# Kernel optimization log

Hardware: AMD Instinct MI355X
Metric: run time of the kernel (lower is better)

## Reference

```python
import math
import jax, jax.numpy as jnp
import numpy as np

E = 256
HEADS = 8
WS = 8
BN_EPS = 1e-5


def pos_encoding_2d(embed_dim, H, W):
    d_half = embed_dim // 2
    div = jnp.exp(jnp.arange(0, d_half, 2, dtype=jnp.float32) * (-math.log(10000.0) / d_half))
    ang_h = jnp.arange(H, dtype=jnp.float32)[:, None] * div[None, :]  # [H, d_half//2]
    pe_h = jnp.zeros((H, d_half), jnp.float32).at[:, 0::2].set(jnp.sin(ang_h)).at[:, 1::2].set(jnp.cos(ang_h))
    ang_w = jnp.arange(W, dtype=jnp.float32)[:, None] * div[None, :]
    pe_w = jnp.zeros((W, d_half), jnp.float32).at[:, 0::2].set(jnp.sin(ang_w)).at[:, 1::2].set(jnp.cos(ang_w))
    pe = jnp.concatenate([
        jnp.broadcast_to(pe_h[:, None, :], (H, W, d_half)),
        jnp.broadcast_to(pe_w[None, :, :], (H, W, d_half)),
    ], axis=-1)  # [H, W, E]
    return jnp.transpose(pe, (2, 0, 1))[None]  # [1, E, H, W]


def window_partition(x, ws):
    # x: [B, E, H, W] -> [B*Hn*Wn, ws*ws, E]
    B, e, H, W = x.shape
    Hn, Wn = H // ws, W // ws
    x = x.reshape(B, e, Hn, ws, Wn, ws)
    x = jnp.transpose(x, (0, 2, 4, 3, 5, 1))  # [B, Hn, Wn, ws, ws, E]
    return x.reshape(B * Hn * Wn, ws * ws, e)


def window_reverse(x, B, H, W, ws):
    Hn, Wn = H // ws, W // ws
    e = x.shape[-1]
    x = x.reshape(B, Hn, Wn, ws, ws, e)
    x = jnp.transpose(x, (0, 5, 1, 3, 2, 4))  # [B, E, Hn, ws, Wn, ws]
    return x.reshape(B, e, H, W)


def setup_inputs() -> dict:
    key = jax.random.key(0)
    ks = jax.random.split(key, 16)
    B, H, W = 8, 128, 128
    in_ch = (512, 256, 256)
    s = lambda fan: 1.0 / np.sqrt(fan)
    return {
        "x5": jax.random.normal(ks[0], (B, in_ch[0], H, W), jnp.float32),
        "d1": jax.random.normal(ks[1], (B, in_ch[1], H, W), jnp.float32),
        "d2": jax.random.normal(ks[2], (B, in_ch[2], H, W), jnp.float32),
        "kp_w": jax.random.normal(ks[3], (E, in_ch[0]), jnp.float32) * s(in_ch[0]),
        "qp_w": jax.random.normal(ks[4], (E, in_ch[1]), jnp.float32) * s(in_ch[1]),
        "vp_w": jax.random.normal(ks[5], (E, in_ch[2]), jnp.float32) * s(in_ch[2]),
        "sp_w": jax.random.normal(ks[6], (E, in_ch[1]), jnp.float32) * s(in_ch[1]),
        "in_proj_w": jax.random.normal(ks[7], (3 * E, E), jnp.float32) * s(E),
        "in_proj_b": jnp.zeros((3 * E,), jnp.float32),
        "out_proj_w": jax.random.normal(ks[8], (E, E), jnp.float32) * s(E),
        "out_proj_b": jnp.zeros((E,), jnp.float32),
        "post_w": jax.random.normal(ks[9], (E, 2 * E, 3, 3), jnp.float32) * s(2 * E * 9),
        "gamma": jnp.ones((E,), jnp.float32),
        "beta": jnp.zeros((E,), jnp.float32),
    }


def reference(x5, d1, d2, kp_w, qp_w, vp_w, sp_w, in_proj_w, in_proj_b,
              out_proj_w, out_proj_b, post_w, gamma, beta):
    B, _, H, W = d1.shape
    pe = pos_encoding_2d(E, H, W)

    # 1x1 projections + positional encoding
    q = jnp.einsum('bchw,ec->behw', d1, qp_w) + pe
    k = jnp.einsum('bchw,ec->behw', x5, kp_w) + pe
    v = jnp.einsum('bchw,ec->behw', d2, vp_w) + pe

    # window partition -> [N, L, E]
    qw = window_partition(q, WS)
    kw = window_partition(k, WS)
    vw = window_partition(v, WS)
    N, L, _ = qw.shape
    hd = E // HEADS

    Wq, Wk, Wv = in_proj_w[:E], in_proj_w[E:2 * E], in_proj_w[2 * E:]
    bq, bk, bv = in_proj_b[:E], in_proj_b[E:2 * E], in_proj_b[2 * E:]
    qh = (qw @ Wq.T + bq).reshape(N, L, HEADS, hd)
    kh = (kw @ Wk.T + bk).reshape(N, L, HEADS, hd)
    vh = (vw @ Wv.T + bv).reshape(N, L, HEADS, hd)

    scale = 1.0 / math.sqrt(hd)
    scores = jnp.einsum('nqhd,nkhd->nhqk', qh, kh) * scale  # [N, heads, L, L]
    attn = jax.nn.softmax(scores, axis=-1)
    o = jnp.einsum('nhqk,nkhd->nqhd', attn, vh).reshape(N, L, E)
    o = o @ out_proj_w.T + out_proj_b

    attn_out = window_reverse(o, B, H, W, WS)  # [B, E, H, W]
    skip = jnp.einsum('bchw,ec->behw', d1, sp_w)

    y = jnp.concatenate([attn_out, skip], axis=1)  # [B, 2E, H, W]
    y = jax.lax.conv_general_dilated(
        y, post_w, window_strides=(1, 1), padding=((1, 1), (1, 1)),
        dimension_numbers=('NCHW', 'OIHW', 'NCHW'))
    # BatchNorm2d, training-mode batch statistics
    mean = jnp.mean(y, axis=(0, 2, 3), keepdims=True)
    var = jnp.var(y, axis=(0, 2, 3), keepdims=True)
    y = (y - mean) * jax.lax.rsqrt(var + BN_EPS)
    y = y * gamma[None, :, None, None] + beta[None, :, None, None]
    return jax.nn.relu(y)
```

## Files before the change

kernel.cpp:

```cpp
#include <hip/hip_runtime.h>
#include <cstdio>
#include <cmath>

typedef __attribute__((ext_vector_type(8))) short bf16x8;
typedef __attribute__((ext_vector_type(4))) float f32x4;

#define MFMA16(a, b, c) __builtin_amdgcn_mfma_f32_16x16x32_bf16((a), (b), (c), 0, 0, 0)

#define WSO_PE    0u
#define WSO_PWQS  65536u
#define WSO_PWK   (WSO_PWQS + 262144u)
#define WSO_PWV   (WSO_PWK + 262144u)
#define WSO_WOP   (WSO_PWV + 131072u)
#define WSO_WC    (WSO_WOP + 131072u)
#define WSO_TB    (WSO_WC + 2359296u)
#define WSO_QH    (WSO_TB + 786432u)
#define WSO_KH    (WSO_QH + 67108864u)
#define WSO_VT    (WSO_KH + 67108864u)
#define WSO_YT    (WSO_VT + 67108864u)
#define WSO_SUMS  (WSO_YT + 134217728u)
#define WSO_SC    (WSO_SUMS + 2048u)
#define WSO_TOTAL (WSO_SC + 2048u)

#define SMEM_CONV 152064
#define SMEM_PROJ 66048

__device__ __forceinline__ unsigned short f2b(float x) {
  unsigned int u = __builtin_bit_cast(unsigned int, x);
  u += 0x7fffu + ((u >> 16) & 1u);
  return (unsigned short)(u >> 16);
}

__device__ __forceinline__ float b2f(unsigned short x) {
  return __builtin_bit_cast(float, ((unsigned int)x) << 16);
}

__device__ __forceinline__ bf16x8 rd8(const unsigned short* s, int row, int stride, int k) {
  return *reinterpret_cast<const bf16x8*>(s + row * stride + (k ^ ((row & 7) << 3)));
}

__device__ __forceinline__ unsigned pack_idx(unsigned oc, unsigned ch, unsigned Mdiv) {
  unsigned kc = ch >> 6, moG = oc >> 6, rt = (oc >> 4) & 3, ks = (ch >> 5) & 1;
  unsigned l = (oc & 15) | (((ch >> 3) & 3) << 4), e = ch & 7;
  return ((((kc * Mdiv + moG) * 4 + rt) * 2 + ks) * 64 + l) * 8 + e;
}

__global__ void k_prep(const float* __restrict__ spw, const float* __restrict__ opw,
                       const float* __restrict__ postw,
                       float* __restrict__ peT, unsigned short* __restrict__ pwqs,
                       unsigned short* __restrict__ wop, unsigned short* __restrict__ wc) {
  unsigned id = blockIdx.x * 256u + threadIdx.x;
  if (id < 16384u) {
    int p = id >> 7, j = id & 127;
    float div = expf(-9.210340371976184f * (float)(j & ~1) * (1.0f / 128.0f));
    float ang = (float)p * div;
    peT[id] = (j & 1) ? cosf(ang) : sinf(ang);
    return;
  }
  unsigned i = id - 16384u;
  if (i >= 1310720u) return;
  if (i < 65536u) {
    unsigned oc = i >> 8, ch = i & 255u;
    pwqs[pack_idx(oc + 256u, ch, 8u)] = f2b(spw[i]);
  } else if (i < 131072u) {
    wop[i - 65536u] = f2b(opw[i - 65536u]);
  } else {
    unsigned r = i - 131072u;
    unsigned e = r & 7u, l = (r >> 3) & 63u, rt = (r >> 9) & 3u;
    unsigned idx3 = r >> 11;
    unsigned tap = idx3 % 9u, q = idx3 / 9u;
    unsigned ocb = q & 3u, cc = q >> 2;
    unsigned oc = ocb * 64u + rt * 16u + (l & 15u);
    unsigned ic = cc * 32u + (l >> 4) * 8u + e;
    wc[r] = f2b(postw[(oc * 512u + ic) * 9u + tap]);
  }
}

__global__ void k_fold(const float* __restrict__ qpw, const float* __restrict__ kpw,
                       const float* __restrict__ vpw, const float* __restrict__ inw,
                       const float* __restrict__ inb, const float* __restrict__ peT,
                       unsigned short* __restrict__ pwqs, unsigned short* __restrict__ pwk,
                       unsigned short* __restrict__ pwv, unsigned short* __restrict__ tbh) {
  __shared__ float wrow[256];
  const int tid = threadIdx.x, bid = blockIdx.x;
  if (bid < 768) {
    int m = bid >> 8;
    int e2 = bid & 255;
    wrow[tid] = inw[(m * 256 + e2) * 256 + tid];
    __syncthreads();
    if (m == 1) {
      float a0 = 0.f, a1 = 0.f;
      for (int e = 0; e < 256; ++e) {
        float s = wrow[e];
        a0 = fmaf(s, kpw[e * 512 + tid], a0);
        a1 = fmaf(s, kpw[e * 512 + 256 + tid], a1);
      }
      pwk[pack_idx(e2, tid, 4u)] = f2b(a0);
      pwk[pack_idx(e2, tid + 256, 4u)] = f2b(a1);
    } else {
      const float* pw = (m == 0) ? qpw : vpw;
      float a0 = 0.f;
      for (int e = 0; e < 256; ++e) a0 = fmaf(wrow[e], pw[e * 256 + tid], a0);
      if (m == 0) pwqs[pack_idx(e2, tid, 8u)] = f2b(a0);
      else        pwv[pack_idx(e2, tid, 4u)] = f2b(a0);
    }
  } else {
    int r = bid - 768;
    int t = r >> 7, p = r & 127;
    if (tid < 128) wrow[tid] = peT[p * 128 + tid];
    __syncthreads();
    int woff = (t >> 1) * 256, joff = (t & 1) * 128;
    float acc = (t & 1) ? 0.f : inb[woff + tid];
    const float* wr = inw + (size_t)(woff + tid) * 256 + joff;
    for (int j = 0; j < 128; ++j) acc = fmaf(wrow[j], wr[j], acc);
    tbh[t * 32768 + p * 256 + tid] = f2b(acc);
  }
}

__device__ __forceinline__ void gemm4x4(f32x4 acc[4][4], const unsigned short* __restrict__ wA,
                                        int Kw, int kw0, const unsigned short* sB, int strideB,
                                        int nK, int wid, int lane) {
  const int rA = lane & 15;
  const int kq = (lane >> 4) << 3;
  for (int ks = 0; ks < nK; ks += 32) {
    bf16x8 a[4];
#pragma unroll
    for (int rt = 0; rt < 4; ++rt)
      a[rt] = *reinterpret_cast<const bf16x8*>(wA + (wid * 64 + rt * 16 + rA) * Kw + kw0 + ks + kq);
#pragma unroll
    for (int ct = 0; ct < 4; ++ct) {
      bf16x8 bb = rd8(sB, ct * 16 + rA, strideB, ks + kq);
#pragma unroll
      for (int rt = 0; rt < 4; ++rt) acc[rt][ct] = MFMA16(a[rt], bb, acc[rt][ct]);
    }
  }
}

__device__ __forceinline__ void epi_global(unsigned short* __restrict__ y_t, const f32x4 acc[4][4],
                                           const float* __restrict__ bias, int chOff,
                                           int b, int h0, int w0, int wid, int lane) {
#pragma unroll
  for (int rt = 0; rt < 4; ++rt) {
    int e0 = wid * 64 + rt * 16 + ((lane >> 4) << 2);
    float4 bs = bias ? *reinterpret_cast<const float4*>(bias + e0) : make_float4(0.f, 0.f, 0.f, 0.f);
    int ch = chOff + e0;
#pragma unroll
    for (int ct = 0; ct < 4; ++ct) {
      int tok = ct * 16 + (lane & 15);
      int r = tok >> 3, cpx = tok & 7;
      long gy = ((((long)(b * 16 + (ch >> 5)) * 128 + (h0 + r)) * 128 + (w0 + cpx)) << 5) + (ch & 31);
      ushort4 pk;
      pk.x = f2b(acc[rt][ct][0] + bs.x);
      pk.y = f2b(acc[rt][ct][1] + bs.y);
      pk.z = f2b(acc[rt][ct][2] + bs.z);
      pk.w = f2b(acc[rt][ct][3] + bs.w);
      *reinterpret_cast<ushort4*>(y_t + gy) = pk;
    }
  }
}

__launch_bounds__(512, 4)
__global__ void k_proj(const float* __restrict__ x5, const float* __restrict__ d1,
                       const float* __restrict__ d2,
                       const unsigned short* __restrict__ pwqs, const unsigned short* __restrict__ pwk,
                       const unsigned short* __restrict__ pwv, const unsigned short* __restrict__ tbh,
                       unsigned short* __restrict__ qh, unsigned short* __restrict__ kh,
                       unsigned short* __restrict__ vt, unsigned short* __restrict__ y_t) {
  extern __shared__ unsigned short sB[];
  __shared__ unsigned short tbl[6144];
  const int tid = threadIdx.x, l = tid & 63, wv = tid >> 6;
  const int l15 = l & 15, gq = l >> 4;
  const int braw = blockIdx.x;
  const int bid = (braw & 7) * 384 + (braw >> 3);
  const int unit = bid >> 10, tile = bid & 1023;
  const int wt = tile & 7, hs = (tile >> 3) & 15, b = tile >> 7;
  const int h0 = hs * 8, w0 = wt * 16;
  const int win = wv & 1, og = wv >> 1;

  const float* src; const unsigned short* wf; int Mdiv, Cin;
  if (unit == 0)      { src = d1; wf = pwqs; Mdiv = 8; Cin = 256; }
  else if (unit == 1) { src = x5; wf = pwk;  Mdiv = 4; Cin = 512; }
  else                { src = d2; wf = pwv;  Mdiv = 4; Cin = 256; }

  {
    const unsigned short* tA = tbh + (unit * 2) * 32768;
    const unsigned short* tB = tA + 32768;
#pragma unroll
    for (int k = 0; k < 3; ++k) {
      int v = tid + (k << 9);
      int row24 = v >> 6, ch4 = (v & 63) << 2;
      const unsigned short* s = (row24 < 8) ? (tA + (h0 + row24) * 256 + ch4)
                                            : (tB + (w0 + row24 - 8) * 256 + ch4);
      *reinterpret_cast<ushort4*>(&tbl[row24 * 256 + ch4]) = *reinterpret_cast<const ushort4*>(s);
    }
  }

  const int tokq = tid & 31, ch16 = tid >> 5;
  const long pxoff = (long)(h0 + (tokq >> 2)) * 128 + w0 + (tokq & 3) * 4;
  const int rowb = ((tokq & 3) >> 1) * 64 + (tokq >> 2) * 8 + (tokq & 1) * 4;

  auto stage_half = [&](int chOff, int c2) {
    float4 pv[8];
    const float* sp = src + (((long)(b * Cin + chOff + ch16 * 16 + c2 * 8)) << 14) + pxoff;
#pragma unroll
    for (int uu = 0; uu < 8; ++uu)
      pv[uu] = *reinterpret_cast<const float4*>(sp + ((long)uu << 14));
    const int bb = ch16 * 2 + c2, group = bb >> 3, g = bb & 7;
    const int colbase = (group << 6) + ((((g & 1) << 2) | (g >> 1)) << 3);
#pragma unroll
    for (int e = 0; e < 4; ++e) {
      bf16x8 pk;
#pragma unroll
      for (int uu = 0; uu < 8; ++uu)
        ((unsigned short*)&pk)[uu] = f2b(reinterpret_cast<const float*>(&pv[uu])[e]);
      *reinterpret_cast<bf16x8*>(&sB[(rowb + e) * 258 + colbase]) = pk;
    }
  };

  int bRow[4];
#pragma unroll
  for (int ct = 0; ct < 4; ++ct) bRow[ct] = (win * 64 + ct * 16 + l15) * 258;
  const int p0 = (((gq & 1) << 2) | (gq >> 1)) << 3;

  const f32x4 vz = {0.f, 0.f, 0.f, 0.f};
  f32x4 acc[4][4];

  auto zacc = [&]() {
#pragma unroll
    for (int rt = 0; rt < 4; ++rt)
#pragma unroll
      for (int ct = 0; ct < 4; ++ct) acc[rt][ct] = vz;
  };

  auto run_tile = [&](int moG, int kc0, int kcn) {
    for (int kc = kc0; kc < kc0 + kcn; ++kc) {
      const unsigned short* pa = wf + (((kc * Mdiv + moG) << 12) | (l << 3));
      const int kcL = (kc & 3) << 6;
#pragma unroll
      for (int ksi = 0; ksi < 2; ++ksi) {
        bf16x8 a[4];
#pragma unroll
        for (int rt = 0; rt < 4; ++rt)
          a[rt] = *reinterpret_cast<const bf16x8*>(pa + ((rt * 2 + ksi) << 9));
#pragma unroll
        for (int ct = 0; ct < 4; ++ct) {
          bf16x8 bb = *reinterpret_cast<const bf16x8*>(&sB[bRow[ct] + kcL + p0 + ksi * 16]);
#pragma unroll
          for (int rt = 0; rt < 4; ++rt) acc[rt][ct] = MFMA16(a[rt], bb, acc[rt][ct]);
        }
      }
    }
  };

  const int win_g = ((b * 16 + hs) << 4) + wt * 2 + win;

  auto epi_qk = [&](int moG, int which) {
    unsigned short* dst = (which == 0 ? qh : kh) + ((size_t)win_g << 14);
#pragma unroll
    for (int rt = 0; rt < 4; ++rt) {
      int oc = moG * 64 + rt * 16 + gq * 4;
#pragma unroll
      for (int ct = 0; ct < 4; ++ct) {
        int wtok = ct * 16 + l15;
        ushort4 av = *reinterpret_cast<const ushort4*>(&tbl[(wtok >> 3) * 256 + oc]);
        ushort4 bv = *reinterpret_cast<const ushort4*>(
            &tbl[(8 + win * 8 + (wtok & 7)) * 256 + oc]);
        ushort4 pk;
        pk.x = f2b(acc[rt][ct][0] + b2f(av.x) + b2f(bv.x));
        pk.y = f2b(acc[rt][ct][1] + b2f(av.y) + b2f(bv.y));
        pk.z = f2b(acc[rt][ct][2] + b2f(av.z) + b2f(bv.z));
        pk.w = f2b(acc[rt][ct][3] + b2f(av.w) + b2f(bv.w));
        *reinterpret_cast<ushort4*>(dst + ((oc >> 5) << 11) + (wtok << 5) + (oc & 31)) = pk;
      }
    }
  };

  if (unit == 0) {
    stage_half(0, 0); stage_half(0, 1);
    __syncthreads();
    zacc();
    run_tile(og, 0, 4);
    epi_qk(og, 0);
    zacc();
    run_tile(4 + og, 0, 4);
    {
      const int moG = 4 + og;
#pragma unroll
      for (int rt = 0; rt < 4; ++rt) {
        int ch = moG * 64 + rt * 16 + gq * 4;
        int cc = ch >> 5;
#pragma unroll
        for (int ct = 0; ct < 4; ++ct) {
          int wtok = ct * 16 + l15;
          int h = h0 + (wtok >> 3), wgl = w0 + win * 8 + (wtok & 7);
          long gy = ((((long)(b * 16 + cc) * 128 + h) * 128 + wgl) << 5) + (ch & 31);
          ushort4 pk;
          pk.x = f2b(acc[rt][ct][0]);
          pk.y = f2b(acc[rt][ct][1]);
          pk.z = f2b(acc[rt][ct][2]);
          pk.w = f2b(acc[rt][ct][3]);
          *reinterpret_cast<ushort4*>(y_t + gy) = pk;
        }
      }
    }
  } else if (unit == 1) {
    stage_half(0, 0); stage_half(0, 1);
    __syncthreads();
    zacc();
    run_tile(og, 0, 4);
    __syncthreads();
    stage_half(256, 0); stage_half(256, 1);
    __syncthreads();
    run_tile(og, 4, 4);
    epi_qk(og, 1);
  } else {
    stage_half(0, 0); stage_half(0, 1);
    __syncthreads();
    zacc();
    run_tile(og, 0, 4);
    {
      unsigned short* dst = vt + ((size_t)win_g << 14);
#pragma unroll
      for (int rt = 0; rt < 4; ++rt) {
        int oc = og * 64 + rt * 16 + gq * 4;
        int hd = oc >> 5, chb = oc & 31;
#pragma unroll
        for (int ct = 0; ct < 4; ++ct) {
          int wtok = ct * 16 + l15;
          ushort4 av = *reinterpret_cast<const ushort4*>(&tbl[(wtok >> 3) * 256 + oc]);
          ushort4 bv = *reinterpret_cast<const ushort4*>(
              &tbl[(8 + win * 8 + (wtok & 7)) * 256 + oc]);
          const unsigned short* avp = reinterpret_cast<const unsigned short*>(&av);
          const unsigned short* bvp = reinterpret_cast<const unsigned short*>(&bv);
#pragma unroll
          for (int j = 0; j < 4; ++j)
            dst[(hd << 11) + (chb + j) * 64 + wtok] = f2b(acc[rt][ct][j] + b2f(avp[j]) + b2f(bvp[j]));
        }
      }
    }
  }
}

__launch_bounds__(256, 3)
__global__ void k_wattn(const unsigned short* __restrict__ qh, const unsigned short* __restrict__ kh,
                        const unsigned short* __restrict__ vt, const unsigned short* __restrict__ wop,
                        const float* __restrict__ out_b, unsigned short* __restrict__ y_t) {
  __shared__ unsigned short Pb[4096];
  __shared__ unsigned short bufO[16384];
  const int tid = threadIdx.x, lane = tid & 63, wid = tid >> 6;
  const int gq = lane >> 4, l15 = lane & 15, kq = gq << 3;
  const int bid = blockIdx.x;
  const int win = ((bid & 7) << 8) | (bid >> 3);
  const int b = win >> 8, wh = (win >> 4) & 15, ww = win & 15;
  const int h0 = wh * 8, w0 = ww * 8;

  const unsigned short* qw = qh + ((size_t)win << 14);
  const unsigned short* kw = kh + ((size_t)win << 14);
  const unsigned short* vw = vt + ((size_t)win << 14);

  const f32x4 vz = {0.f, 0.f, 0.f, 0.f};
  const float scl = 0.17677669529663687f;
  f32x4 o0[8], o1[8];
#pragma unroll
  for (int h = 0; h < 8; ++h) { o0[h] = vz; o1[h] = vz; }

#pragma unroll
  for (int hd = 0; hd < 8; ++hd) {
    const unsigned short* qb = qw + (hd << 11);
    const unsigned short* kb = kw + (hd << 11);
    const unsigned short* vb = vw + (hd << 11);
    bf16x8 aq = *reinterpret_cast<const bf16x8*>(qb + ((wid * 16 + l15) << 5) + kq);
    f32x4 sv[4];
#pragma unroll
    for (int ct = 0; ct < 4; ++ct) {
      bf16x8 bk = *reinterpret_cast<const bf16x8*>(kb + ((ct * 16 + l15) << 5) + kq);
      sv[ct] = MFMA16(aq, bk, vz);
    }
    float pr[4][4];
#pragma unroll
    for (int j = 0; j < 4; ++j) {
      float mx = fmaxf(fmaxf(sv[0][j], sv[1][j]), fmaxf(sv[2][j], sv[3][j])) * scl;
#pragma unroll
      for (int m = 8; m >= 1; m >>= 1) mx = fmaxf(mx, __shfl_xor(mx, m));
      float sum = 0.f;
#pragma unroll
      for (int ct = 0; ct < 4; ++ct) {
        float p = __expf(sv[ct][j] * scl - mx);
        pr[ct][j] = p;
        sum += p;
      }
#pragma unroll
      for (int m = 8; m >= 1; m >>= 1) sum += __shfl_xor(sum, m);
      float inv = 1.f / sum;
#pragma unroll
      for (int ct = 0; ct < 4; ++ct) pr[ct][j] *= inv;
    }
#pragma unroll
    for (int ct = 0; ct < 4; ++ct)
#pragma unroll
      for (int j = 0; j < 4; ++j) {
        int q = wid * 16 + gq * 4 + j;
        int kt = ct * 16 + l15;
        Pb[q * 64 + (kt ^ ((q & 7) << 3))] = f2b(pr[ct][j]);
      }
#pragma unroll
    for (int ks = 0; ks < 64; ks += 32) {
      bf16x8 bp = rd8(Pb, wid * 16 + l15, 64, ks + kq);
      bf16x8 a0 = *reinterpret_cast<const bf16x8*>(vb + (l15 << 6) + ks + kq);
      bf16x8 a1 = *reinterpret_cast<const bf16x8*>(vb + ((16 + l15) << 6) + ks + kq);
      o0[hd] = MFMA16(a0, bp, o0[hd]);
      o1[hd] = MFMA16(a1, bp, o1[hd]);
    }
  }

  {
    int tok = wid * 16 + l15;
    int sw = (tok & 7) << 3;
#pragma unroll
    for (int hd = 0; hd < 8; ++hd)
#pragma unroll
      for (int rt = 0; rt < 2; ++rt) {
        f32x4 ov = rt ? o1[hd] : o0[hd];
        int ch0 = hd * 32 + rt * 16 + gq * 4;
        ushort4 pk;
        pk.x = f2b(ov[0]); pk.y = f2b(ov[1]); pk.z = f2b(ov[2]); pk.w = f2b(ov[3]);
        *reinterpret_cast<ushort4*>(&bufO[tok * 256 + (ch0 ^ sw)]) = pk;
      }
  }
  __syncthreads();

  f32x4 accA[4][4];
#pragma unroll
  for (int i = 0; i < 4; ++i)
#pragma unroll
    for (int j = 0; j < 4; ++j) accA[i][j] = vz;
  gemm4x4(accA, wop, 256, 0, bufO, 256, 256, wid, lane);
  epi_global(y_t, accA, out_b, 0, b, h0, w0, wid, lane);
}

__device__ __forceinline__ void patch_load(const unsigned short* __restrict__ y_t,
                                           int b, int cc, int h0, int w0, int tid, uint4* pv) {
#pragma unroll
  for (int k = 0; k < 5; ++k) {
    int s = tid + (k << 9);
    uint4 v = make_uint4(0u, 0u, 0u, 0u);
    if (s < 2448) {
      int pr = (s * 482) >> 16;
      int rem = s - pr * 136;
      int pcpx = rem >> 2, g = rem & 3;
      int hh = h0 + pr - 1, wp = w0 + pcpx - 1;
      if ((unsigned)hh < 128u && (unsigned)wp < 128u)
        v = *reinterpret_cast<const uint4*>(
            y_t + ((((long)(b * 16 + cc) * 128 + hh) * 128 + wp) << 5) + (g << 3));
    }
    pv[k] = v;
  }
}

__device__ __forceinline__ void patch_store(unsigned short* buf, int tid, const uint4* pv) {
#pragma unroll
  for (int k = 0; k < 5; ++k) {
    int s = tid + (k << 9);
    if (s < 2448) {
      int pr = (s * 482) >> 16;
      int rem = s - pr * 136;
      int pcpx = rem >> 2, g = rem & 3;
      int pidx = pr * 34 + pcpx;
      *reinterpret_cast<uint4*>(buf + (pidx << 5) + ((g ^ ((pidx >> 1) & 3)) << 3)) = pv[k];
    }
  }
}

__device__ __forceinline__ void stage_A(const unsigned short* __restrict__ wA, int cc, int ocb,
                                        unsigned short* dstBase, int tid) {
  const unsigned short* src = wA + (size_t)(cc * 4 + ocb) * 18432 + tid * 8;
  unsigned short* dst = dstBase + tid * 8;
#pragma unroll
  for (int k = 0; k < 4; ++k) {
    __builtin_amdgcn_global_load_lds(
        (const __attribute__((address_space(1))) unsigned int*)(src + k * 4096),
        (__attribute__((address_space(3))) unsigned int*)(dst + k * 4096), 16, 0, 0);
  }
  if (tid < 256)
    __builtin_amdgcn_global_load_lds(
        (const __attribute__((address_space(1))) unsigned int*)(src + 16384),
        (__attribute__((address_space(3))) unsigned int*)(dst + 16384), 16, 0, 0);
}

__launch_bounds__(512, 2)
__global__ void k_conv(const unsigned short* __restrict__ y_t, const unsigned short* __restrict__ wc,
                       float* __restrict__ out) {
  extern __shared__ unsigned short cs[];
  unsigned short* Pb0 = cs;
  unsigned short* Pb1 = cs + 19584;
  unsigned short* Ab0 = cs + 39168;
  unsigned short* Ab1 = cs + 57600;

  const int tid = threadIdx.x, lane = tid & 63, pxg = tid >> 6;
  const int gq = lane >> 4, l15 = lane & 15;
  const int bi = ((int)blockIdx.x & 7) * 128 + ((int)blockIdx.x >> 3);
  const int ocb = bi & 3, wb = (bi >> 2) & 3, hb = (bi >> 4) & 7, b = bi >> 7;
  const int h0 = hb * 16, w0 = wb * 32;

  const f32x4 vz = {0.f, 0.f, 0.f, 0.f};
  f32x4 acc[4][4];
#pragma unroll
  for (int rt = 0; rt < 4; ++rt)
#pragma unroll
    for (int ct = 0; ct < 4; ++ct) acc[rt][ct] = vz;

  uint4 pv[5];
  patch_load(y_t, b, 0, h0, w0, tid, pv);
  stage_A(wc, 0, ocb, Ab0, tid);
  patch_store(Pb0, tid, pv);
  __syncthreads();

#pragma unroll 1
  for (int cc = 0; cc < 16; ++cc) {
    const unsigned short* pb = (cc & 1) ? Pb1 : Pb0;
    const unsigned short* pa = (cc & 1) ? Ab1 : Ab0;
    if (cc < 15) {
      patch_load(y_t, b, cc + 1, h0, w0, tid, pv);
      stage_A(wc, cc + 1, ocb, (cc & 1) ? Ab0 : Ab1, tid);
    }

#pragma unroll
    for (int kx = 0; kx < 3; ++kx) {
      bf16x8 bfr[4][2];
#pragma unroll
      for (int r = 0; r < 4; ++r)
#pragma unroll
        for (int ws = 0; ws < 2; ++ws) {
          int pidx = (pxg * 2 + r) * 34 + ws * 16 + l15 + kx;
          bfr[r][ws] = *reinterpret_cast<const bf16x8*>(
              pb + (pidx << 5) + ((gq ^ ((pidx >> 1) & 3)) << 3));
        }
      bf16x8 afr[3][4];
#pragma unroll
      for (int ky = 0; ky < 3; ++ky)
#pragma unroll
        for (int rt = 0; rt < 4; ++rt)
          afr[ky][rt] = *reinterpret_cast<const bf16x8*>(
              pa + (((ky * 3 + kx) * 4 + rt) << 9) + lane * 8);
#pragma unroll
      for (int ky = 0; ky < 3; ++ky)
#pragma unroll
        for (int ct = 0; ct < 4; ++ct) {
          int r = (ct >> 1) + ky, ws = ct & 1;
#pragma unroll
          for (int rt = 0; rt < 4; ++rt)
            acc[rt][ct] = MFMA16(afr[ky][rt], bfr[r][ws], acc[rt][ct]);
        }
    }

    if (cc < 15) patch_store((cc & 1) ? Pb0 : Pb1, tid, pv);
    __syncthreads();
  }

#pragma unroll
  for (int rt = 0; rt < 4; ++rt) {
    int oc0 = ocb * 64 + rt * 16 + gq * 4;
#pragma unroll
    for (int ct = 0; ct < 4; ++ct) {
      int hh = h0 + pxg * 2 + (ct >> 1), wp = w0 + ((ct & 1) << 4) + l15;
      long base = (((long)(b * 256 + oc0)) * 128 + hh) * 128 + wp;
#pragma unroll
      for (int j = 0; j < 4; ++j) out[base + (long)j * 16384] = acc[rt][ct][j];
    }
  }
}

__global__ void k_stats(const float* __restrict__ out, float* __restrict__ sums) {
  __shared__ float s1[256], s2[256];
  int c = blockIdx.x, tid = threadIdx.x;
  float a1 = 0.f, a2 = 0.f;
  for (int bb = 0; bb < 8; ++bb) {
    const float4* p = reinterpret_cast<const float4*>(out + ((long)(bb * 256 + c)) * 16384);
    for (int i = tid; i < 4096; i += 256) {
      float4 v = p[i];
      a1 += v.x + v.y + v.z + v.w;
      a2 += v.x * v.x + v.y * v.y + v.z * v.z + v.w * v.w;
    }
  }
  s1[tid] = a1; s2[tid] = a2;
  __syncthreads();
  for (int s = 128; s > 0; s >>= 1) {
    if (tid < s) { s1[tid] += s1[tid + s]; s2[tid] += s2[tid + s]; }
    __syncthreads();
  }
  if (tid == 0) { sums[c] = s1[0]; sums[256 + c] = s2[0]; }
}

__global__ void k_final(const float* __restrict__ sums, const float* __restrict__ gamma,
                        const float* __restrict__ beta, float* __restrict__ sc) {
  int c = threadIdx.x;
  float mean = sums[c] * (1.f / 131072.f);
  float var = sums[256 + c] * (1.f / 131072.f) - mean * mean;
  float s = gamma[c] * rsqrtf(var + 1e-5f);
  sc[c] = s;
  sc[256 + c] = beta[c] - mean * s;
}

__global__ void k_apply(float* __restrict__ out, const float* __restrict__ sc) {
  const long n4 = 33554432 / 4;
  for (long i4 = (long)blockIdx.x * 256 + threadIdx.x; i4 < n4; i4 += (long)gridDim.x * 256) {
    float4 v = reinterpret_cast<float4*>(out)[i4];
    int c = (int)((i4 >> 12) & 255);
    float s = sc[c], sh = sc[256 + c];
    v.x = fmaxf(v.x * s + sh, 0.f);
    v.y = fmaxf(v.y * s + sh, 0.f);
    v.z = fmaxf(v.z * s + sh, 0.f);
    v.w = fmaxf(v.w * s + sh, 0.f);
    reinterpret_cast<float4*>(out)[i4] = v;
  }
}

extern "C" void kernel_launch(void* const* d_in, const int* in_sizes, int n_in,
                              void* d_out, int out_size, void* d_ws, size_t ws_size,
                              hipStream_t stream) {
  const float* x5 = (const float*)d_in[0];
  const float* d1 = (const float*)d_in[1];
  const float* d2 = (const float*)d_in[2];
  const float* kp = (const float*)d_in[3];
  const float* qp = (const float*)d_in[4];
  const float* vp = (const float*)d_in[5];
  const float* spw = (const float*)d_in[6];
  const float* inw = (const float*)d_in[7];
  const float* inb = (const float*)d_in[8];
  const float* opw = (const float*)d_in[9];
  const float* opb = (const float*)d_in[10];
  const float* pw = (const float*)d_in[11];
  const float* gamma = (const float*)d_in[12];
  const float* beta = (const float*)d_in[13];

  if (ws_size < (size_t)WSO_TOTAL) {
    fprintf(stderr, "kernel_launch: ws too small: %zu < %u\n", ws_size, WSO_TOTAL);
    return;
  }

  char* ws = (char*)d_ws;
  float* peT = (float*)(ws + WSO_PE);
  unsigned short* pwqs = (unsigned short*)(ws + WSO_PWQS);
  unsigned short* pwk = (unsigned short*)(ws + WSO_PWK);
  unsigned short* pwv = (unsigned short*)(ws + WSO_PWV);
  unsigned short* w_op = (unsigned short*)(ws + WSO_WOP);
  unsigned short* w_c = (unsigned short*)(ws + WSO_WC);
  unsigned short* tbh = (unsigned short*)(ws + WSO_TB);
  unsigned short* qh = (unsigned short*)(ws + WSO_QH);
  unsigned short* kh = (unsigned short*)(ws + WSO_KH);
  unsigned short* vt = (unsigned short*)(ws + WSO_VT);
  unsigned short* y_t = (unsigned short*)(ws + WSO_YT);
  float* sums = (float*)(ws + WSO_SUMS);
  float* sc = (float*)(ws + WSO_SC);

  hipFuncSetAttribute(reinterpret_cast<const void*>(k_conv),
                      hipFuncAttributeMaxDynamicSharedMemorySize, SMEM_CONV);
  hipFuncSetAttribute(reinterpret_cast<const void*>(k_proj),
                      hipFuncAttributeMaxDynamicSharedMemorySize, SMEM_PROJ);

  k_prep<<<5184, 256, 0, stream>>>(spw, opw, pw, peT, pwqs, w_op, w_c);
  k_fold<<<1536, 256, 0, stream>>>(qp, kp, vp, inw, inb, peT, pwqs, pwk, pwv, tbh);
  k_proj<<<3072, 512, SMEM_PROJ, stream>>>(x5, d1, d2, pwqs, pwk, pwv, tbh, qh, kh, vt, y_t);
  k_wattn<<<2048, 256, 0, stream>>>(qh, kh, vt, w_op, opb, y_t);
  k_conv<<<1024, 512, SMEM_CONV, stream>>>(y_t, w_c, (float*)d_out);
  k_stats<<<256, 256, 0, stream>>>((const float*)d_out, sums);
  k_final<<<1, 256, 0, stream>>>(sums, gamma, beta, sc);
  k_apply<<<2048, 256, 0, stream>>>((float*)d_out, sc);
}
```

Before: 792.1 us.

## Fuse BN statistics into conv epilogue and retile projection kernel per image row

Batch-norm sum and sum-of-squares are now reduced inside the conv kernel's epilogue with wave shuffles and shared memory, then written as per-block partials that k_final adds up. This removes the separate k_stats pass that re-read the whole fp32 output. The projection kernel is also retiled: each block now handles one full 128-pixel image row with a new weight packing and XOR-swizzled shared staging, and it reads the position tables straight from global memory instead of a shared copy. The risks are a serial 256-step reduction loop in k_final, scalar bf16 stores to shared memory, and a changed access pattern for the source loads.

```diff
diff --git a/kernel.cpp b/kernel.cpp
--- a/kernel.cpp
+++ b/kernel.cpp
@@ -20,10 +20,12 @@
 #define WSO_YT    (WSO_VT + 67108864u)
 #define WSO_SUMS  (WSO_YT + 134217728u)
 #define WSO_SC    (WSO_SUMS + 2048u)
-#define WSO_TOTAL (WSO_SC + 2048u)
+#define WSO_PS    (WSO_SC + 2048u)
+#define WSO_PSQ   (WSO_PS + 262144u)
+#define WSO_TOTAL (WSO_PSQ + 262144u)
 
 #define SMEM_CONV 152064
-#define SMEM_PROJ 66048
+#define SMEM_PROJ 67584
 
 __device__ __forceinline__ unsigned short f2b(float x) {
   unsigned int u = __builtin_bit_cast(unsigned int, x);
@@ -39,10 +41,10 @@
   return *reinterpret_cast<const bf16x8*>(s + row * stride + (k ^ ((row & 7) << 3)));
 }
 
-__device__ __forceinline__ unsigned pack_idx(unsigned oc, unsigned ch, unsigned Mdiv) {
-  unsigned kc = ch >> 6, moG = oc >> 6, rt = (oc >> 4) & 3, ks = (ch >> 5) & 1;
+__device__ __forceinline__ unsigned pack2(unsigned oc, unsigned ch, unsigned NOG) {
+  unsigned kc = ch >> 5, og = oc >> 5, rt = (oc >> 4) & 1;
   unsigned l = (oc & 15) | (((ch >> 3) & 3) << 4), e = ch & 7;
-  return ((((kc * Mdiv + moG) * 4 + rt) * 2 + ks) * 64 + l) * 8 + e;
+  return (((kc * NOG + og) * 2 + rt) * 64 + l) * 8 + e;
 }
 
 __global__ void k_prep(const float* __restrict__ spw, const float* __restrict__ opw,
@@ -61,7 +63,7 @@
   if (i >= 1310720u) return;
   if (i < 65536u) {
     unsigned oc = i >> 8, ch = i & 255u;
-    pwqs[pack_idx(oc + 256u, ch, 8u)] = f2b(spw[i]);
+    pwqs[pack2(oc + 256u, ch, 16u)] = f2b(spw[i]);
   } else if (i < 131072u) {
     wop[i - 65536u] = f2b(opw[i - 65536u]);
   } else {
@@ -95,14 +97,14 @@
         a0 = fmaf(s, kpw[e * 512 + tid], a0);
         a1 = fmaf(s, kpw[e * 512 + 256 + tid], a1);
       }
-      pwk[pack_idx(e2, tid, 4u)] = f2b(a0);
-      pwk[pack_idx(e2, tid + 256, 4u)] = f2b(a1);
+      pwk[pack2(e2, tid, 8u)] = f2b(a0);
+      pwk[pack2(e2, tid + 256, 8u)] = f2b(a1);
     } else {
       const float* pw = (m == 0) ? qpw : vpw;
       float a0 = 0.f;
       for (int e = 0; e < 256; ++e) a0 = fmaf(wrow[e], pw[e * 256 + tid], a0);
-      if (m == 0) pwqs[pack_idx(e2, tid, 8u)] = f2b(a0);
-      else        pwv[pack_idx(e2, tid, 4u)] = f2b(a0);
+      if (m == 0) pwqs[pack2(e2, tid, 16u)] = f2b(a0);
+      else        pwv[pack2(e2, tid, 8u)] = f2b(a0);
     }
   } else {
     int r = bid - 768;
@@ -167,177 +169,175 @@
                        unsigned short* __restrict__ qh, unsigned short* __restrict__ kh,
                        unsigned short* __restrict__ vt, unsigned short* __restrict__ y_t) {
   extern __shared__ unsigned short sB[];
-  __shared__ unsigned short tbl[6144];
   const int tid = threadIdx.x, l = tid & 63, wv = tid >> 6;
   const int l15 = l & 15, gq = l >> 4;
-  const int braw = blockIdx.x;
-  const int bid = (braw & 7) * 384 + (braw >> 3);
-  const int unit = bid >> 10, tile = bid & 1023;
-  const int wt = tile & 7, hs = (tile >> 3) & 15, b = tile >> 7;
-  const int h0 = hs * 8, w0 = wt * 16;
-  const int win = wv & 1, og = wv >> 1;
-
-  const float* src; const unsigned short* wf; int Mdiv, Cin;
-  if (unit == 0)      { src = d1; wf = pwqs; Mdiv = 8; Cin = 256; }
-  else if (unit == 1) { src = x5; wf = pwk;  Mdiv = 4; Cin = 512; }
-  else                { src = d2; wf = pwv;  Mdiv = 4; Cin = 256; }
-
-  {
-    const unsigned short* tA = tbh + (unit * 2) * 32768;
-    const unsigned short* tB = tA + 32768;
-#pragma unroll
-    for (int k = 0; k < 3; ++k) {
-      int v = tid + (k << 9);
-      int row24 = v >> 6, ch4 = (v & 63) << 2;
-      const unsigned short* s = (row24 < 8) ? (tA + (h0 + row24) * 256 + ch4)
-                                            : (tB + (w0 + row24 - 8) * 256 + ch4);
-      *reinterpret_cast<ushort4*>(&tbl[row24 * 256 + ch4]) = *reinterpret_cast<const ushort4*>(s);
-    }
-  }
-
-  const int tokq = tid & 31, ch16 = tid >> 5;
-  const long pxoff = (long)(h0 + (tokq >> 2)) * 128 + w0 + (tokq & 3) * 4;
-  const int rowb = ((tokq & 3) >> 1) * 64 + (tokq >> 2) * 8 + (tokq & 1) * 4;
-
-  auto stage_half = [&](int chOff, int c2) {
-    float4 pv[8];
-    const float* sp = src + (((long)(b * Cin + chOff + ch16 * 16 + c2 * 8)) << 14) + pxoff;
-#pragma unroll
-    for (int uu = 0; uu < 8; ++uu)
-      pv[uu] = *reinterpret_cast<const float4*>(sp + ((long)uu << 14));
-    const int bb = ch16 * 2 + c2, group = bb >> 3, g = bb & 7;
-    const int colbase = (group << 6) + ((((g & 1) << 2) | (g >> 1)) << 3);
-#pragma unroll
-    for (int e = 0; e < 4; ++e) {
-      bf16x8 pk;
-#pragma unroll
-      for (int uu = 0; uu < 8; ++uu)
-        ((unsigned short*)&pk)[uu] = f2b(reinterpret_cast<const float*>(&pv[uu])[e]);
-      *reinterpret_cast<bf16x8*>(&sB[(rowb + e) * 258 + colbase]) = pk;
-    }
+  const int bid = blockIdx.x;
+  const int unit = bid % 3, tile = bid / 3;
+  const int h0 = tile & 127, b = tile >> 7;
+  const int tokG = wv & 1, ogPair = wv >> 1;
+  const int chsub = tid >> 4, pxg = (tid & 15) << 3;
+  const int winRow = (b * 16 + (h0 >> 3)) << 4;
+
+  auto ld2 = [&](const float* src, int Cin, int kc, float4& v0, float4& v1) {
+    int ch = kc * 32 + chsub;
+    const float* g = src + (((long)(b * Cin + ch)) << 14) + h0 * 128 + pxg;
+    v0 = *reinterpret_cast<const float4*>(g);
+    v1 = *reinterpret_cast<const float4*>(g + 4);
   };
-
-  int bRow[4];
-#pragma unroll
-  for (int ct = 0; ct < 4; ++ct) bRow[ct] = (win * 64 + ct * 16 + l15) * 258;
-  const int p0 = (((gq & 1) << 2) | (gq >> 1)) << 3;
+  auto wr2 = [&](int kc, const float4& v0, const float4& v1) {
+    int ch = kc * 32 + chsub, chL = ch & 255;
+    int group = chL >> 6, gg = (chL >> 3) & 7, pos = chL & 7;
+    const float* f0 = reinterpret_cast<const float*>(&v0);
+    const float* f1 = reinterpret_cast<const float*>(&v1);
+#pragma unroll
+    for (int i = 0; i < 4; ++i) {
+      int px = pxg + i;
+      sB[px * 264 + (group << 6) + (((gg ^ (px & 7))) << 3) + pos] = f2b(f0[i]);
+    }
+#pragma unroll
+    for (int i = 0; i < 4; ++i) {
+      int px = pxg + 4 + i;
+      sB[px * 264 + (group << 6) + (((gg ^ (px & 7))) << 3) + pos] = f2b(f1[i]);
+    }
+  };
+  auto stageN = [&](const float* src, int Cin, int kc0, int n) {
+    float4 a0, a1, b0, b1;
+    ld2(src, Cin, kc0, a0, a1);
+#pragma unroll 1
+    for (int k = 0; k < n; ++k) {
+      if (k + 1 < n) ld2(src, Cin, kc0 + k + 1, b0, b1);
+      wr2(kc0 + k, a0, a1);
+      a0 = b0; a1 = b1;
+    }
+  };
 
   const f32x4 vz = {0.f, 0.f, 0.f, 0.f};
-  f32x4 acc[4][4];
-
+  f32x4 acc[2][2][4];
   auto zacc = [&]() {
 #pragma unroll
-    for (int rt = 0; rt < 4; ++rt)
-#pragma unroll
-      for (int ct = 0; ct < 4; ++ct) acc[rt][ct] = vz;
+    for (int sl = 0; sl < 2; ++sl)
+#pragma unroll
+      for (int rt = 0; rt < 2; ++rt)
+#pragma unroll
+        for (int ct = 0; ct < 4; ++ct) acc[sl][rt][ct] = vz;
   };
 
-  auto run_tile = [&](int moG, int kc0, int kcn) {
+  auto run = [&](const unsigned short* wf, int NOG, int ogBase, int kc0, int kcn) {
+#pragma unroll 1
     for (int kc = kc0; kc < kc0 + kcn; ++kc) {
-      const unsigned short* pa = wf + (((kc * Mdiv + moG) << 12) | (l << 3));
-      const int kcL = (kc & 3) << 6;
-#pragma unroll
-      for (int ksi = 0; ksi < 2; ++ksi) {
-        bf16x8 a[4];
-#pragma unroll
-        for (int rt = 0; rt < 4; ++rt)
-          a[rt] = *reinterpret_cast<const bf16x8*>(pa + ((rt * 2 + ksi) << 9));
+      const int kcL = kc & 7;
+      const int chb = kcL * 32 + gq * 8;
+      const int group = chb >> 6, gg = (chb >> 3) & 7;
+      bf16x8 bb[4];
+#pragma unroll
+      for (int ct = 0; ct < 4; ++ct) {
+        int px = tokG * 64 + ct * 16 + l15;
+        bb[ct] = *reinterpret_cast<const bf16x8*>(
+            &sB[px * 264 + (group << 6) + ((gg ^ (px & 7)) << 3)]);
+      }
+#pragma unroll
+      for (int sl = 0; sl < 2; ++sl) {
+        int og = ogBase + ogPair * 2 + sl;
+        const unsigned short* pa = wf + (((((kc * NOG + og) << 7) + l)) << 3);
+        bf16x8 a0 = *reinterpret_cast<const bf16x8*>(pa);
+        bf16x8 a1 = *reinterpret_cast<const bf16x8*>(pa + 512);
 #pragma unroll
         for (int ct = 0; ct < 4; ++ct) {
-          bf16x8 bb = *reinterpret_cast<const bf16x8*>(&sB[bRow[ct] + kcL + p0 + ksi * 16]);
-#pragma unroll
-          for (int rt = 0; rt < 4; ++rt) acc[rt][ct] = MFMA16(a[rt], bb, acc[rt][ct]);
+          acc[sl][0][ct] = MFMA16(a0, bb[ct], acc[sl][0][ct]);
+          acc[sl][1][ct] = MFMA16(a1, bb[ct], acc[sl][1][ct]);
         }
       }
     }
   };
 
-  const int win_g = ((b * 16 + hs) << 4) + wt * 2 + win;
-
-  auto epi_qk = [&](int moG, int which) {
-    unsigned short* dst = (which == 0 ? qh : kh) + ((size_t)win_g << 14);
-#pragma unroll
-    for (int rt = 0; rt < 4; ++rt) {
-      int oc = moG * 64 + rt * 16 + gq * 4;
-#pragma unroll
-      for (int ct = 0; ct < 4; ++ct) {
-        int wtok = ct * 16 + l15;
-        ushort4 av = *reinterpret_cast<const ushort4*>(&tbl[(wtok >> 3) * 256 + oc]);
-        ushort4 bv = *reinterpret_cast<const ushort4*>(
-            &tbl[(8 + win * 8 + (wtok & 7)) * 256 + oc]);
-        ushort4 pk;
-        pk.x = f2b(acc[rt][ct][0] + b2f(av.x) + b2f(bv.x));
-        pk.y = f2b(acc[rt][ct][1] + b2f(av.y) + b2f(bv.y));
-        pk.z = f2b(acc[rt][ct][2] + b2f(av.z) + b2f(bv.z));
-        pk.w = f2b(acc[rt][ct][3] + b2f(av.w) + b2f(bv.w));
-        *reinterpret_cast<ushort4*>(dst + ((oc >> 5) << 11) + (wtok << 5) + (oc & 31)) = pk;
+  auto epi_qk = [&](unsigned short* dstBase, const unsigned short* tA, const unsigned short* tB) {
+#pragma unroll
+    for (int sl = 0; sl < 2; ++sl) {
+#pragma unroll
+      for (int rt = 0; rt < 2; ++rt) {
+        int oc = (ogPair * 2 + sl) * 32 + rt * 16 + gq * 4;
+        int hd = oc >> 5, c31 = oc & 31;
+        ushort4 av = *reinterpret_cast<const ushort4*>(&tA[h0 * 256 + oc]);
+#pragma unroll
+        for (int ct = 0; ct < 4; ++ct) {
+          int px = tokG * 64 + ct * 16 + l15;
+          ushort4 bv = *reinterpret_cast<const ushort4*>(&tB[px * 256 + oc]);
+          int win = px >> 3, tokw = ((h0 & 7) << 3) | (px & 7);
+          unsigned short* dst = dstBase + ((size_t)(winRow + win) << 14);
+          ushort4 pk;
+          pk.x = f2b(acc[sl][rt][ct][0] + b2f(av.x) + b2f(bv.x));
+          pk.y = f2b(acc[sl][rt][ct][1] + b2f(av.y) + b2f(bv.y));
+          pk.z = f2b(acc[sl][rt][ct][2] + b2f(av.z) + b2f(bv.z));
+          pk.w = f2b(acc[sl][rt][ct][3] + b2f(av.w) + b2f(bv.w));
+          *reinterpret_cast<ushort4*>(dst + (hd << 11) + (tokw << 5) + c31) = pk;
+        }
       }
     }
   };
 
   if (unit == 0) {
-    stage_half(0, 0); stage_half(0, 1);
+    stageN(d1, 256, 0, 8);
     __syncthreads();
     zacc();
-    run_tile(og, 0, 4);
-    epi_qk(og, 0);
+    run(pwqs, 16, 0, 0, 8);
+    epi_qk(qh, tbh, tbh + 32768);
     zacc();
-    run_tile(4 + og, 0, 4);
-    {
-      const int moG = 4 + og;
-#pragma unroll
-      for (int rt = 0; rt < 4; ++rt) {
-        int ch = moG * 64 + rt * 16 + gq * 4;
+    run(pwqs, 16, 8, 0, 8);
+#pragma unroll
+    for (int sl = 0; sl < 2; ++sl)
+#pragma unroll
+      for (int rt = 0; rt < 2; ++rt) {
+        int ch = (8 + ogPair * 2 + sl) * 32 + rt * 16 + gq * 4;
         int cc = ch >> 5;
 #pragma unroll
         for (int ct = 0; ct < 4; ++ct) {
-          int wtok = ct * 16 + l15;
-          int h = h0 + (wtok >> 3), wgl = w0 + win * 8 + (wtok & 7);
-          long gy = ((((long)(b * 16 + cc) * 128 + h) * 128 + wgl) << 5) + (ch & 31);
+          int px = tokG * 64 + ct * 16 + l15;
+          long gy = ((((long)(b * 16 + cc) * 128 + h0) * 128 + px) << 5) + (ch & 31);
           ushort4 pk;
-          pk.x = f2b(acc[rt][ct][0]);
-          pk.y = f2b(acc[rt][ct][1]);
-          pk.z = f2b(acc[rt][ct][2]);
-          pk.w = f2b(acc[rt][ct][3]);
+          pk.x = f2b(acc[sl][rt][ct][0]);
+          pk.y = f2b(acc[sl][rt][ct][1]);
+          pk.z = f2b(acc[sl][rt][ct][2]);
+          pk.w = f2b(acc[sl][rt][ct][3]);
           *reinterpret_cast<ushort4*>(y_t + gy) = pk;
         }
       }
-    }
   } else if (unit == 1) {
-    stage_half(0, 0); stage_half(0, 1);
+    stageN(x5, 512, 0, 8);
     __syncthreads();
     zacc();
-    run_tile(og, 0, 4);
-    __syncthreads();
-    stage_half(256, 0); stage_half(256, 1);
-    __syncthreads();
-    run_tile(og, 4, 4);
-    epi_qk(og, 1);
+    run(pwk, 8, 0, 0, 8);
+    __syncthreads();
+    stageN(x5, 512, 8, 8);
+    __syncthreads();
+    run(pwk, 8, 0, 8, 8);
+    epi_qk(kh, tbh + 65536, tbh + 98304);
   } else {
-    stage_half(0, 0); stage_half(0, 1);
+    stageN(d2, 256, 0, 8);
     __syncthreads();
     zacc();
-    run_tile(og, 0, 4);
-    {
-      unsigned short* dst = vt + ((size_t)win_g << 14);
-#pragma unroll
-      for (int rt = 0; rt < 4; ++rt) {
-        int oc = og * 64 + rt * 16 + gq * 4;
+    run(pwv, 8, 0, 0, 8);
+    const unsigned short* tA = tbh + 131072;
+    const unsigned short* tB = tbh + 163840;
+#pragma unroll
+    for (int sl = 0; sl < 2; ++sl)
+#pragma unroll
+      for (int rt = 0; rt < 2; ++rt) {
+        int oc = (ogPair * 2 + sl) * 32 + rt * 16 + gq * 4;
         int hd = oc >> 5, chb = oc & 31;
+        ushort4 av = *reinterpret_cast<const ushort4*>(&tA[h0 * 256 + oc]);
+        const unsigned short* avp = reinterpret_cast<const unsigned short*>(&av);
 #pragma unroll
         for (int ct = 0; ct < 4; ++ct) {
-          int wtok = ct * 16 + l15;
-          ushort4 av = *reinterpret_cast<const ushort4*>(&tbl[(wtok >> 3) * 256 + oc]);
-          ushort4 bv = *reinterpret_cast<const ushort4*>(
-              &tbl[(8 + win * 8 + (wtok & 7)) * 256 + oc]);
-          const unsigned short* avp = reinterpret_cast<const unsigned short*>(&av);
+          int px = tokG * 64 + ct * 16 + l15;
+          ushort4 bv = *reinterpret_cast<const ushort4*>(&tB[px * 256 + oc]);
           const unsigned short* bvp = reinterpret_cast<const unsigned short*>(&bv);
+          int win = px >> 3, tokw = ((h0 & 7) << 3) | (px & 7);
+          unsigned short* dst = vt + ((size_t)(winRow + win) << 14) + (hd << 11) + tokw;
 #pragma unroll
           for (int j = 0; j < 4; ++j)
-            dst[(hd << 11) + (chb + j) * 64 + wtok] = f2b(acc[rt][ct][j] + b2f(avp[j]) + b2f(bvp[j]));
-        }
-      }
-    }
+            dst[(chb + j) * 64] = f2b(acc[sl][rt][ct][j] + b2f(avp[j]) + b2f(bvp[j]));
+        }
+      }
   }
 }
 
@@ -489,7 +489,8 @@
 
 __launch_bounds__(512, 2)
 __global__ void k_conv(const unsigned short* __restrict__ y_t, const unsigned short* __restrict__ wc,
-                       float* __restrict__ out) {
+                       float* __restrict__ out, float* __restrict__ psum,
+                       float* __restrict__ psq) {
   extern __shared__ unsigned short cs[];
   unsigned short* Pb0 = cs;
   unsigned short* Pb1 = cs + 19584;
@@ -568,34 +569,57 @@
       for (int j = 0; j < 4; ++j) out[base + (long)j * 16384] = acc[rt][ct][j];
     }
   }
-}
-
-__global__ void k_stats(const float* __restrict__ out, float* __restrict__ sums) {
-  __shared__ float s1[256], s2[256];
-  int c = blockIdx.x, tid = threadIdx.x;
-  float a1 = 0.f, a2 = 0.f;
-  for (int bb = 0; bb < 8; ++bb) {
-    const float4* p = reinterpret_cast<const float4*>(out + ((long)(bb * 256 + c)) * 16384);
-    for (int i = tid; i < 4096; i += 256) {
-      float4 v = p[i];
-      a1 += v.x + v.y + v.z + v.w;
-      a2 += v.x * v.x + v.y * v.y + v.z * v.z + v.w * v.w;
-    }
-  }
-  s1[tid] = a1; s2[tid] = a2;
-  __syncthreads();
-  for (int s = 128; s > 0; s >>= 1) {
-    if (tid < s) { s1[tid] += s1[tid + s]; s2[tid] += s2[tid + s]; }
-    __syncthreads();
-  }
-  if (tid == 0) { sums[c] = s1[0]; sums[256 + c] = s2[0]; }
-}
-
-__global__ void k_final(const float* __restrict__ sums, const float* __restrict__ gamma,
-                        const float* __restrict__ beta, float* __restrict__ sc) {
+
+  {
+    float s1v[4][4], s2v[4][4];
+#pragma unroll
+    for (int rt = 0; rt < 4; ++rt)
+#pragma unroll
+      for (int j = 0; j < 4; ++j) {
+        float a = 0.f, q = 0.f;
+#pragma unroll
+        for (int ct = 0; ct < 4; ++ct) { float y = acc[rt][ct][j]; a += y; q += y * y; }
+        s1v[rt][j] = a; s2v[rt][j] = q;
+      }
+#pragma unroll
+    for (int m = 8; m >= 1; m >>= 1)
+#pragma unroll
+      for (int rt = 0; rt < 4; ++rt)
+#pragma unroll
+        for (int j = 0; j < 4; ++j) {
+          s1v[rt][j] += __shfl_xor(s1v[rt][j], m);
+          s2v[rt][j] += __shfl_xor(s2v[rt][j], m);
+        }
+    __shared__ float redS[8][64], redQ[8][64];
+    if (l15 == 0) {
+#pragma unroll
+      for (int rt = 0; rt < 4; ++rt)
+#pragma unroll
+        for (int j = 0; j < 4; ++j) {
+          redS[pxg][rt * 16 + gq * 4 + j] = s1v[rt][j];
+          redQ[pxg][rt * 16 + gq * 4 + j] = s2v[rt][j];
+        }
+    }
+    __syncthreads();
+    if (tid < 64) {
+      float a = 0.f, q = 0.f;
+#pragma unroll
+      for (int w = 0; w < 8; ++w) { a += redS[w][tid]; q += redQ[w][tid]; }
+      int pb2 = bi >> 2;
+      psum[pb2 * 256 + ocb * 64 + tid] = a;
+      psq[pb2 * 256 + ocb * 64 + tid] = q;
+    }
+  }
+}
+
+__global__ void k_final(const float* __restrict__ psum, const float* __restrict__ psq,
+                        const float* __restrict__ gamma, const float* __restrict__ beta,
+                        float* __restrict__ sc) {
   int c = threadIdx.x;
-  float mean = sums[c] * (1.f / 131072.f);
-  float var = sums[256 + c] * (1.f / 131072.f) - mean * mean;
+  float s1 = 0.f, s2 = 0.f;
+  for (int p = 0; p < 256; ++p) { s1 += psum[p * 256 + c]; s2 += psq[p * 256 + c]; }
+  float mean = s1 * (1.f / 131072.f);
+  float var = s2 * (1.f / 131072.f) - mean * mean;
   float s = gamma[c] * rsqrtf(var + 1e-5f);
   sc[c] = s;
   sc[256 + c] = beta[c] - mean * s;
@@ -650,8 +674,9 @@
   unsigned short* kh = (unsigned short*)(ws + WSO_KH);
   unsigned short* vt = (unsigned short*)(ws + WSO_VT);
   unsigned short* y_t = (unsigned short*)(ws + WSO_YT);
-  float* sums = (float*)(ws + WSO_SUMS);
   float* sc = (float*)(ws + WSO_SC);
+  float* psum = (float*)(ws + WSO_PS);
+  float* psq = (float*)(ws + WSO_PSQ);
 
   hipFuncSetAttribute(reinterpret_cast<const void*>(k_conv),
                       hipFuncAttributeMaxDynamicSharedMemorySize, SMEM_CONV);
@@ -662,8 +687,7 @@
   k_fold<<<1536, 256, 0, stream>>>(qp, kp, vp, inw, inb, peT, pwqs, pwk, pwv, tbh);
   k_proj<<<3072, 512, SMEM_PROJ, stream>>>(x5, d1, d2, pwqs, pwk, pwv, tbh, qh, kh, vt, y_t);
   k_wattn<<<2048, 256, 0, stream>>>(qh, kh, vt, w_op, opb, y_t);
-  k_conv<<<1024, 512, SMEM_CONV, stream>>>(y_t, w_c, (float*)d_out);
-  k_stats<<<256, 256, 0, stream>>>((const float*)d_out, sums);
-  k_final<<<1, 256, 0, stream>>>(sums, gamma, beta, sc);
+  k_conv<<<1024, 512, SMEM_CONV, stream>>>(y_t, w_c, (float*)d_out, psum, psq);
+  k_final<<<1, 256, 0, stream>>>(psum, psq, gamma, beta, sc);
   k_apply<<<2048, 256, 0, stream>>>((float*)d_out, sc);
 }
```

Result: faster. 741.1 us (-6.4%).
